# Optimization experiments

Hardware: AMD Instinct MI355X
Metric: run time of the kernel (lower is better)

Reference implementation:

```python
import jax, jax.numpy as jnp
import numpy as np

B, Q, L, D_LLM, D_KEYS = 2, 8, 2048, 768, 64
EPS = 1e-5

def setup_inputs() -> dict:
    key = jax.random.key(0)
    ks = jax.random.split(key, 7)
    s_in = 1.0 / np.sqrt(D_LLM)
    return {
        "info": jax.random.normal(ks[0], (B, Q, L, D_LLM), dtype=jnp.float32),
        "Wq": jax.random.uniform(ks[1], (D_LLM, D_KEYS), jnp.float32, -s_in, s_in),
        "bq": jax.random.uniform(ks[2], (D_KEYS,), jnp.float32, -s_in, s_in),
        "Wk": jax.random.uniform(ks[3], (D_LLM, D_KEYS), jnp.float32, -s_in, s_in),
        "bk": jax.random.uniform(ks[4], (D_KEYS,), jnp.float32, -s_in, s_in),
        "Wv": jax.random.uniform(ks[5], (D_LLM, D_KEYS), jnp.float32, -s_in, s_in),
        "bv": jax.random.uniform(ks[6], (D_KEYS,), jnp.float32, -s_in, s_in),
    }

def reference(info, Wq, bq, Wk, bk, Wv, bv):
    # Projections: [B,Q,L,d_llm] @ [d_llm,d_keys] -> [B,Q,L,E]
    q = info @ Wq + bq
    k = info @ Wk + bk
    v = info @ Wv + bv
    E = q.shape[-1]
    scale = 1.0 / jnp.sqrt(jnp.asarray(E, dtype=q.dtype))
    # Full L x L score tensor per (b,q) slice, as in the original einsum path
    scores = jnp.einsum('bqle,bqme->bqlm', q, k)
    A = jax.nn.softmax(scale * scores, axis=-1)  # dropout is identity at eval
    out = jnp.einsum('bqlm,bqme->bqle', A, v)    # [B,Q,L,E]
    # InstanceNorm2d (no affine): normalize each (b,q) slice over (L,E)
    mu = jnp.mean(out, axis=(2, 3), keepdims=True)
    var = jnp.var(out, axis=(2, 3), keepdims=True)  # biased variance
    return (out - mu) / jnp.sqrt(var + EPS)
```

## Files before the change

kernel.cpp:

```cpp
#include <hip/hip_runtime.h>
#include <math.h>

#define L_SEQ   2048
#define DLLM    768
#define E_DIM   64
#define NSLICE  16
#define EPSV    1e-5f

typedef _Float16 f16;
typedef _Float16 f16x8 __attribute__((ext_vector_type(8)));
typedef _Float16 f16x4 __attribute__((ext_vector_type(4)));
typedef float    f32x4 __attribute__((ext_vector_type(4)));

__global__ __launch_bounds__(256)
void prep_kernel(const float* __restrict__ Wq, const float* __restrict__ bq,
                 const float* __restrict__ Wk, const float* __restrict__ bk,
                 const float* __restrict__ Wv, const float* __restrict__ bv,
                 f16* __restrict__ Wt, float* __restrict__ bias)
{
    int b = blockIdx.x;
    if (b < 192) {
        int sel = b >> 6, c = b & 63;
        const float* W = (sel == 0) ? Wq : (sel == 1) ? Wk : Wv;
        float s = (sel == 0) ? 0.125f : 1.0f;
        for (int kd = threadIdx.x; kd < DLLM; kd += 256)
            Wt[b * DLLM + kd] = (f16)(W[kd * 64 + c] * s);
    } else {
        int t = threadIdx.x;
        if (t < 192) {
            int sel = t >> 6, c = t & 63;
            const float* bb = (sel == 0) ? bq : (sel == 1) ? bk : bv;
            bias[t] = bb[c] * ((sel == 0) ? 0.125f : 1.0f);
        }
    }
}

#define PSTR 72

__global__ __launch_bounds__(256)
void proj_mfma(const float* __restrict__ info, const f16* __restrict__ Wt,
               const float* __restrict__ bias,
               f16* __restrict__ q16, f16* __restrict__ k16, f16* __restrict__ v16)
{
    __shared__ f16 As[128 * PSTR];
    __shared__ f16 Bs[192 * PSTR];

    const int tid = threadIdx.x;
    const int l   = tid & 63;
    const int wid = tid >> 6;
    const int l15 = l & 15, lg = l >> 4;
    const int wm  = (wid >> 1) * 64;
    const int wn  = (wid & 1) * 96;
    const int r0  = blockIdx.x * 128;

    f32x4 acc[4][6];
    #pragma unroll
    for (int i = 0; i < 4; ++i)
        #pragma unroll
        for (int j = 0; j < 6; ++j) acc[i][j] = (f32x4)(0.0f);

    for (int k0 = 0; k0 < DLLM; k0 += 64) {
        __syncthreads();
        #pragma unroll
        for (int u = 0; u < 8; ++u) {
            int f = u * 256 + tid;
            int row = f >> 4, c4 = f & 15;
            float4 v = *reinterpret_cast<const float4*>(
                info + (size_t)(r0 + row) * DLLM + k0 + c4 * 4);
            f16x4 h;
            h[0] = (f16)v.x; h[1] = (f16)v.y; h[2] = (f16)v.z; h[3] = (f16)v.w;
            *reinterpret_cast<f16x4*>(&As[row * PSTR + c4 * 4]) = h;
        }
        #pragma unroll
        for (int u = 0; u < 6; ++u) {
            int f = u * 256 + tid;
            int row = f >> 3, c8 = f & 7;
            f16x8 v = *reinterpret_cast<const f16x8*>(Wt + (size_t)row * DLLM + k0 + c8 * 8);
            *reinterpret_cast<f16x8*>(&Bs[row * PSTR + c8 * 8]) = v;
        }
        __syncthreads();

        #pragma unroll
        for (int kf = 0; kf < 2; ++kf) {
            f16x8 af[4], bf[6];
            #pragma unroll
            for (int mi = 0; mi < 4; ++mi)
                af[mi] = *reinterpret_cast<const f16x8*>(
                    &As[(wm + mi * 16 + l15) * PSTR + kf * 32 + lg * 8]);
            #pragma unroll
            for (int ni = 0; ni < 6; ++ni)
                bf[ni] = *reinterpret_cast<const f16x8*>(
                    &Bs[(wn + ni * 16 + l15) * PSTR + kf * 32 + lg * 8]);
            #pragma unroll
            for (int mi = 0; mi < 4; ++mi)
                #pragma unroll
                for (int ni = 0; ni < 6; ++ni)
                    acc[mi][ni] = __builtin_amdgcn_mfma_f32_16x16x32_f16(
                        af[mi], bf[ni], acc[mi][ni], 0, 0, 0);
        }
    }

    #pragma unroll
    for (int ni = 0; ni < 6; ++ni) {
        int n = wn + ni * 16 + l15;
        float bcol = bias[n];
        int sel = n >> 6, cc = n & 63;
        f16* dst = (sel == 0) ? q16 : (sel == 1) ? k16 : v16;
        #pragma unroll
        for (int mi = 0; mi < 4; ++mi)
            #pragma unroll
            for (int rr = 0; rr < 4; ++rr) {
                int row = r0 + wm + mi * 16 + lg * 4 + rr;
                dst[(size_t)row * E_DIM + cc] = (f16)(acc[mi][ni][rr] + bcol);
            }
    }
}

#define VSTR 72

__global__ __launch_bounds__(256)
void attn_mfma(const f16* __restrict__ q16, const f16* __restrict__ k16,
               const f16* __restrict__ v16, float* __restrict__ att)
{
    __shared__ f16 Vt[64 * VSTR];
    __shared__ f16 Pl[4 * 16 * VSTR];

    const int tid = threadIdx.x;
    const int l   = tid & 63;
    const int wid = tid >> 6;
    const int l15 = l & 15, lg = l >> 4;
    const int slice = blockIdx.y;
    const int m0 = blockIdx.x * 64 + wid * 16;
    const f16* qp = q16 + (size_t)slice * L_SEQ * E_DIM;
    const f16* kp = k16 + (size_t)slice * L_SEQ * E_DIM;
    const f16* vp = v16 + (size_t)slice * L_SEQ * E_DIM;
    f16* P = &Pl[wid * 16 * VSTR];

    f16x8 qf[2];
    #pragma unroll
    for (int kf = 0; kf < 2; ++kf)
        qf[kf] = *reinterpret_cast<const f16x8*>(
            qp + (size_t)(m0 + l15) * E_DIM + kf * 32 + lg * 8);

    f32x4 oacc[4];
    #pragma unroll
    for (int ni = 0; ni < 4; ++ni) oacc[ni] = (f32x4)(0.0f);
    float M[4] = {-1e30f, -1e30f, -1e30f, -1e30f};
    float Lr[4] = {0.f, 0.f, 0.f, 0.f};

    for (int kv0 = 0; kv0 < L_SEQ; kv0 += 64) {
        __syncthreads();

        #pragma unroll
        for (int u = 0; u < 2; ++u) {
            int f  = u * 256 + tid;
            int r  = f >> 3;
            int c8 = f & 7;
            f16x8 h = *reinterpret_cast<const f16x8*>(
                vp + (size_t)(kv0 + r) * E_DIM + c8 * 8);
            int col = r ^ (c8 << 3);
            #pragma unroll
            for (int j = 0; j < 8; ++j)
                Vt[(c8 * 8 + j) * VSTR + col] = h[j];
        }

        f32x4 s[4];
        #pragma unroll
        for (int ni = 0; ni < 4; ++ni) s[ni] = (f32x4)(0.0f);
        #pragma unroll
        for (int kf = 0; kf < 2; ++kf)
            #pragma unroll
            for (int ni = 0; ni < 4; ++ni) {
                f16x8 kb = *reinterpret_cast<const f16x8*>(
                    kp + (size_t)(kv0 + ni * 16 + l15) * E_DIM + kf * 32 + lg * 8);
                s[ni] = __builtin_amdgcn_mfma_f32_16x16x32_f16(qf[kf], kb, s[ni], 0, 0, 0);
            }

        #pragma unroll
        for (int r = 0; r < 4; ++r) {
            float v0 = s[0][r], v1 = s[1][r], v2 = s[2][r], v3 = s[3][r];
            float mx = fmaxf(fmaxf(v0, v1), fmaxf(v2, v3));
            mx = fmaxf(mx, __shfl_xor(mx, 1));
            mx = fmaxf(mx, __shfl_xor(mx, 2));
            mx = fmaxf(mx, __shfl_xor(mx, 4));
            mx = fmaxf(mx, __shfl_xor(mx, 8));
            float mn  = fmaxf(M[r], mx);
            float fsc = __expf(M[r] - mn);
            M[r] = mn;
            float p0 = __expf(v0 - mn), p1 = __expf(v1 - mn);
            float p2 = __expf(v2 - mn), p3 = __expf(v3 - mn);
            int prow = (lg * 4 + r) * VSTR + l15;
            P[prow +  0] = (f16)p0;
            P[prow + 16] = (f16)p1;
            P[prow + 32] = (f16)p2;
            P[prow + 48] = (f16)p3;
            Lr[r] = Lr[r] * fsc + (p0 + p1 + p2 + p3);
            oacc[0][r] *= fsc; oacc[1][r] *= fsc;
            oacc[2][r] *= fsc; oacc[3][r] *= fsc;
        }

        __syncthreads();

        #pragma unroll
        for (int kf = 0; kf < 2; ++kf) {
            f16x8 pa = *reinterpret_cast<const f16x8*>(
                &P[l15 * VSTR + kf * 32 + lg * 8]);
            #pragma unroll
            for (int ni = 0; ni < 4; ++ni) {
                int e   = ni * 16 + l15;
                int col = (kf * 32 + lg * 8) ^ ((e >> 3) << 3);
                f16x8 vb = *reinterpret_cast<const f16x8*>(&Vt[e * VSTR + col]);
                oacc[ni] = __builtin_amdgcn_mfma_f32_16x16x32_f16(pa, vb, oacc[ni], 0, 0, 0);
            }
        }
    }

    #pragma unroll
    for (int r = 0; r < 4; ++r) {
        float lt = Lr[r];
        lt += __shfl_xor(lt, 1);
        lt += __shfl_xor(lt, 2);
        lt += __shfl_xor(lt, 4);
        lt += __shfl_xor(lt, 8);
        float inv = 1.f / lt;
        size_t row = (size_t)slice * L_SEQ + m0 + lg * 4 + r;
        #pragma unroll
        for (int ni = 0; ni < 4; ++ni)
            att[row * E_DIM + ni * 16 + l15] = oacc[ni][r] * inv;
    }
}

__global__ __launch_bounds__(256)
void stats_kernel(const float* __restrict__ att, float* __restrict__ parts)
{
    const int slice = blockIdx.x >> 4;
    const int part  = blockIdx.x & 15;
    const int tid = threadIdx.x;
    const size_t base = (size_t)slice * L_SEQ * E_DIM + (size_t)part * 8192;
    float s = 0.f, sq = 0.f;
    #pragma unroll
    for (int it = 0; it < 8; ++it) {
        float4 v = *reinterpret_cast<const float4*>(att + base + (size_t)(it * 256 + tid) * 4);
        s  += v.x + v.y + v.z + v.w;
        sq += v.x * v.x + v.y * v.y + v.z * v.z + v.w * v.w;
    }
    for (int m = 1; m < 64; m <<= 1) {
        s  += __shfl_xor(s,  m);
        sq += __shfl_xor(sq, m);
    }
    __shared__ float red[8];
    const int wid = tid >> 6;
    if ((tid & 63) == 0) { red[wid * 2] = s; red[wid * 2 + 1] = sq; }
    __syncthreads();
    if (tid == 0) {
        parts[slice * 32 + part * 2]     = red[0] + red[2] + red[4] + red[6];
        parts[slice * 32 + part * 2 + 1] = red[1] + red[3] + red[5] + red[7];
    }
}

__global__ __launch_bounds__(256)
void apply_kernel(float* __restrict__ att, const float* __restrict__ parts)
{
    const int i4 = blockIdx.x * 256 + threadIdx.x;
    const size_t fl = (size_t)i4 * 4;
    const int slice = (int)(fl >> 17);
    float S = 0.f, SQ = 0.f;
    #pragma unroll
    for (int p = 0; p < 16; ++p) {
        S  += parts[slice * 32 + p * 2];
        SQ += parts[slice * 32 + p * 2 + 1];
    }
    const float N = (float)(L_SEQ * E_DIM);
    float mean = S / N;
    float var  = SQ / N - mean * mean;
    float inv  = rsqrtf(var + EPSV);
    float4 v = *reinterpret_cast<const float4*>(att + fl);
    float4 o;
    o.x = (v.x - mean) * inv;
    o.y = (v.y - mean) * inv;
    o.z = (v.z - mean) * inv;
    o.w = (v.w - mean) * inv;
    *reinterpret_cast<float4*>(att + fl) = o;
}

extern "C" void kernel_launch(void* const* d_in, const int* in_sizes, int n_in,
                              void* d_out, int out_size, void* d_ws, size_t ws_size,
                              hipStream_t stream)
{
    const float* info = (const float*)d_in[0];
    const float* Wq   = (const float*)d_in[1];
    const float* bq   = (const float*)d_in[2];
    const float* Wk   = (const float*)d_in[3];
    const float* bk   = (const float*)d_in[4];
    const float* Wv   = (const float*)d_in[5];
    const float* bv   = (const float*)d_in[6];

    char* ws = (char*)d_ws;
    f16*   Wt    = (f16*)(ws);
    float* bias  = (float*)(ws + 294912);
    float* parts = (float*)(ws + 295936);
    f16*   q16   = (f16*)(ws + 1048576);
    f16*   k16   = (f16*)(ws + 5242880);
    f16*   v16   = (f16*)(ws + 9437184);
    float* att   = (float*)d_out;

    prep_kernel<<<193, 256, 0, stream>>>(Wq, bq, Wk, bk, Wv, bv, Wt, bias);
    proj_mfma<<<256, 256, 0, stream>>>(info, Wt, bias, q16, k16, v16);
    attn_mfma<<<dim3(L_SEQ / 64, NSLICE), 256, 0, stream>>>(q16, k16, v16, att);
    stats_kernel<<<256, 256, 0, stream>>>(att, parts);
    apply_kernel<<<2048, 256, 0, stream>>>(att, parts);
}
```

Baseline: 270.8 us.

## Store V transposed, drop LDS staging and block syncs, register-prefetch projection

```diff
diff --git a/kernel.cpp b/kernel.cpp
--- a/kernel.cpp
+++ b/kernel.cpp
@@ -35,135 +35,151 @@
     }
 }
 
-#define PSTR 72
-
 __global__ __launch_bounds__(256)
 void proj_mfma(const float* __restrict__ info, const f16* __restrict__ Wt,
                const float* __restrict__ bias,
-               f16* __restrict__ q16, f16* __restrict__ k16, f16* __restrict__ v16)
-{
-    __shared__ f16 As[128 * PSTR];
-    __shared__ f16 Bs[192 * PSTR];
-
+               f16* __restrict__ q16, f16* __restrict__ k16, f16* __restrict__ vT)
+{
     const int tid = threadIdx.x;
     const int l   = tid & 63;
     const int wid = tid >> 6;
     const int l15 = l & 15, lg = l >> 4;
-    const int wm  = (wid >> 1) * 64;
-    const int wn  = (wid & 1) * 96;
-    const int r0  = blockIdx.x * 128;
-
-    f32x4 acc[4][6];
-    #pragma unroll
-    for (int i = 0; i < 4; ++i)
-        #pragma unroll
-        for (int j = 0; j < 6; ++j) acc[i][j] = (f32x4)(0.0f);
-
-    for (int k0 = 0; k0 < DLLM; k0 += 64) {
-        __syncthreads();
-        #pragma unroll
-        for (int u = 0; u < 8; ++u) {
-            int f = u * 256 + tid;
-            int row = f >> 4, c4 = f & 15;
-            float4 v = *reinterpret_cast<const float4*>(
-                info + (size_t)(r0 + row) * DLLM + k0 + c4 * 4);
-            f16x4 h;
-            h[0] = (f16)v.x; h[1] = (f16)v.y; h[2] = (f16)v.z; h[3] = (f16)v.w;
-            *reinterpret_cast<f16x4*>(&As[row * PSTR + c4 * 4]) = h;
-        }
-        #pragma unroll
-        for (int u = 0; u < 6; ++u) {
-            int f = u * 256 + tid;
-            int row = f >> 3, c8 = f & 7;
-            f16x8 v = *reinterpret_cast<const f16x8*>(Wt + (size_t)row * DLLM + k0 + c8 * 8);
-            *reinterpret_cast<f16x8*>(&Bs[row * PSTR + c8 * 8]) = v;
-        }
-        __syncthreads();
-
+    const int w   = blockIdx.x * 4 + wid;
+    const int rt  = w >> 1;
+    const int ch  = w & 1;
+    const int r0  = rt * 32;
+    const int n0  = ch * 96;
+
+    f32x4 acc[2][6];
+    #pragma unroll
+    for (int mi = 0; mi < 2; ++mi)
+        #pragma unroll
+        for (int ni = 0; ni < 6; ++ni) acc[mi][ni] = (f32x4)(0.0f);
+
+    const float* abase[2];
+    #pragma unroll
+    for (int mi = 0; mi < 2; ++mi)
+        abase[mi] = info + (size_t)(r0 + mi * 16 + l15) * DLLM + lg * 8;
+    const f16* bbase[6];
+    #pragma unroll
+    for (int ni = 0; ni < 6; ++ni)
+        bbase[ni] = Wt + (size_t)(n0 + ni * 16 + l15) * DLLM + lg * 8;
+
+    float4 alo[2][2][2], ahi[2][2][2];
+
+    #pragma unroll
+    for (int mi = 0; mi < 2; ++mi)
         #pragma unroll
         for (int kf = 0; kf < 2; ++kf) {
-            f16x8 af[4], bf[6];
-            #pragma unroll
-            for (int mi = 0; mi < 4; ++mi)
-                af[mi] = *reinterpret_cast<const f16x8*>(
-                    &As[(wm + mi * 16 + l15) * PSTR + kf * 32 + lg * 8]);
-            #pragma unroll
-            for (int ni = 0; ni < 6; ++ni)
-                bf[ni] = *reinterpret_cast<const f16x8*>(
-                    &Bs[(wn + ni * 16 + l15) * PSTR + kf * 32 + lg * 8]);
-            #pragma unroll
-            for (int mi = 0; mi < 4; ++mi)
+            alo[0][mi][kf] = *reinterpret_cast<const float4*>(abase[mi] + kf * 32);
+            ahi[0][mi][kf] = *reinterpret_cast<const float4*>(abase[mi] + kf * 32 + 4);
+        }
+
+    #pragma unroll
+    for (int ks = 0; ks < 12; ++ks) {
+        const int cur = ks & 1, nxt = cur ^ 1;
+        const int k0 = ks * 64;
+        if (ks < 11) {
+            #pragma unroll
+            for (int mi = 0; mi < 2; ++mi)
+                #pragma unroll
+                for (int kf = 0; kf < 2; ++kf) {
+                    alo[nxt][mi][kf] = *reinterpret_cast<const float4*>(
+                        abase[mi] + k0 + 64 + kf * 32);
+                    ahi[nxt][mi][kf] = *reinterpret_cast<const float4*>(
+                        abase[mi] + k0 + 64 + kf * 32 + 4);
+                }
+        }
+        f16x8 bf[6][2];
+        #pragma unroll
+        for (int ni = 0; ni < 6; ++ni)
+            #pragma unroll
+            for (int kf = 0; kf < 2; ++kf)
+                bf[ni][kf] = *reinterpret_cast<const f16x8*>(bbase[ni] + k0 + kf * 32);
+        f16x8 af[2][2];
+        #pragma unroll
+        for (int mi = 0; mi < 2; ++mi)
+            #pragma unroll
+            for (int kf = 0; kf < 2; ++kf) {
+                float4 lo = alo[cur][mi][kf], hi = ahi[cur][mi][kf];
+                f16x8 h;
+                h[0] = (f16)lo.x; h[1] = (f16)lo.y; h[2] = (f16)lo.z; h[3] = (f16)lo.w;
+                h[4] = (f16)hi.x; h[5] = (f16)hi.y; h[6] = (f16)hi.z; h[7] = (f16)hi.w;
+                af[mi][kf] = h;
+            }
+        #pragma unroll
+        for (int kf = 0; kf < 2; ++kf)
+            #pragma unroll
+            for (int mi = 0; mi < 2; ++mi)
                 #pragma unroll
                 for (int ni = 0; ni < 6; ++ni)
                     acc[mi][ni] = __builtin_amdgcn_mfma_f32_16x16x32_f16(
-                        af[mi], bf[ni], acc[mi][ni], 0, 0, 0);
-        }
+                        af[mi][kf], bf[ni][kf], acc[mi][ni], 0, 0, 0);
     }
 
     #pragma unroll
     for (int ni = 0; ni < 6; ++ni) {
-        int n = wn + ni * 16 + l15;
-        float bcol = bias[n];
-        int sel = n >> 6, cc = n & 63;
-        f16* dst = (sel == 0) ? q16 : (sel == 1) ? k16 : v16;
-        #pragma unroll
-        for (int mi = 0; mi < 4; ++mi)
-            #pragma unroll
-            for (int rr = 0; rr < 4; ++rr) {
-                int row = r0 + wm + mi * 16 + lg * 4 + rr;
-                dst[(size_t)row * E_DIM + cc] = (f16)(acc[mi][ni][rr] + bcol);
-            }
-    }
-}
-
-#define VSTR 72
+        const int nb  = n0 + ni * 16;
+        const int n   = nb + l15;
+        const int sel = nb >> 6;
+        const int cc  = (nb & 63) + l15;
+        const float bcol = bias[n];
+        if (sel < 2) {
+            f16* dst = (sel == 0) ? q16 : k16;
+            #pragma unroll
+            for (int mi = 0; mi < 2; ++mi)
+                #pragma unroll
+                for (int rr = 0; rr < 4; ++rr) {
+                    int r = r0 + mi * 16 + lg * 4 + rr;
+                    dst[(size_t)r * E_DIM + cc] = (f16)(acc[mi][ni][rr] + bcol);
+                }
+        } else {
+            #pragma unroll
+            for (int mi = 0; mi < 2; ++mi) {
+                int rb    = r0 + mi * 16 + lg * 4;
+                int slice = rb >> 11;
+                int lloc  = rb & 2047;
+                f16x4 v4;
+                #pragma unroll
+                for (int rr = 0; rr < 4; ++rr) v4[rr] = (f16)(acc[mi][ni][rr] + bcol);
+                *reinterpret_cast<f16x4*>(
+                    vT + (size_t)slice * E_DIM * L_SEQ + (size_t)cc * L_SEQ + lloc) = v4;
+            }
+        }
+    }
+}
+
+#define PSTRD 72
 
 __global__ __launch_bounds__(256)
 void attn_mfma(const f16* __restrict__ q16, const f16* __restrict__ k16,
-               const f16* __restrict__ v16, float* __restrict__ att)
-{
-    __shared__ f16 Vt[64 * VSTR];
-    __shared__ f16 Pl[4 * 16 * VSTR];
+               const f16* __restrict__ vT, float* __restrict__ att)
+{
+    __shared__ f16 Pl[4 * 16 * PSTRD];
 
     const int tid = threadIdx.x;
     const int l   = tid & 63;
     const int wid = tid >> 6;
     const int l15 = l & 15, lg = l >> 4;
     const int slice = blockIdx.y;
-    const int m0 = blockIdx.x * 64 + wid * 16;
+    const int q0 = blockIdx.x * 64 + wid * 16;
     const f16* qp = q16 + (size_t)slice * L_SEQ * E_DIM;
     const f16* kp = k16 + (size_t)slice * L_SEQ * E_DIM;
-    const f16* vp = v16 + (size_t)slice * L_SEQ * E_DIM;
-    f16* P = &Pl[wid * 16 * VSTR];
+    const f16* vp = vT  + (size_t)slice * E_DIM * L_SEQ;
+    f16* P = &Pl[wid * 16 * PSTRD];
 
     f16x8 qf[2];
     #pragma unroll
     for (int kf = 0; kf < 2; ++kf)
         qf[kf] = *reinterpret_cast<const f16x8*>(
-            qp + (size_t)(m0 + l15) * E_DIM + kf * 32 + lg * 8);
+            qp + (size_t)(q0 + l15) * E_DIM + kf * 32 + lg * 8);
 
     f32x4 oacc[4];
     #pragma unroll
-    for (int ni = 0; ni < 4; ++ni) oacc[ni] = (f32x4)(0.0f);
-    float M[4] = {-1e30f, -1e30f, -1e30f, -1e30f};
-    float Lr[4] = {0.f, 0.f, 0.f, 0.f};
+    for (int ei = 0; ei < 4; ++ei) oacc[ei] = (f32x4)(0.0f);
+    float M = -1e30f, Lr = 0.f;
 
     for (int kv0 = 0; kv0 < L_SEQ; kv0 += 64) {
-        __syncthreads();
-
-        #pragma unroll
-        for (int u = 0; u < 2; ++u) {
-            int f  = u * 256 + tid;
-            int r  = f >> 3;
-            int c8 = f & 7;
-            f16x8 h = *reinterpret_cast<const f16x8*>(
-                vp + (size_t)(kv0 + r) * E_DIM + c8 * 8);
-            int col = r ^ (c8 << 3);
-            #pragma unroll
-            for (int j = 0; j < 8; ++j)
-                Vt[(c8 * 8 + j) * VSTR + col] = h[j];
-        }
-
         f32x4 s[4];
         #pragma unroll
         for (int ni = 0; ni < 4; ++ni) s[ni] = (f32x4)(0.0f);
@@ -173,60 +189,62 @@
             for (int ni = 0; ni < 4; ++ni) {
                 f16x8 kb = *reinterpret_cast<const f16x8*>(
                     kp + (size_t)(kv0 + ni * 16 + l15) * E_DIM + kf * 32 + lg * 8);
-                s[ni] = __builtin_amdgcn_mfma_f32_16x16x32_f16(qf[kf], kb, s[ni], 0, 0, 0);
-            }
-
-        #pragma unroll
-        for (int r = 0; r < 4; ++r) {
-            float v0 = s[0][r], v1 = s[1][r], v2 = s[2][r], v3 = s[3][r];
-            float mx = fmaxf(fmaxf(v0, v1), fmaxf(v2, v3));
-            mx = fmaxf(mx, __shfl_xor(mx, 1));
-            mx = fmaxf(mx, __shfl_xor(mx, 2));
-            mx = fmaxf(mx, __shfl_xor(mx, 4));
-            mx = fmaxf(mx, __shfl_xor(mx, 8));
-            float mn  = fmaxf(M[r], mx);
-            float fsc = __expf(M[r] - mn);
-            M[r] = mn;
-            float p0 = __expf(v0 - mn), p1 = __expf(v1 - mn);
-            float p2 = __expf(v2 - mn), p3 = __expf(v3 - mn);
-            int prow = (lg * 4 + r) * VSTR + l15;
-            P[prow +  0] = (f16)p0;
-            P[prow + 16] = (f16)p1;
-            P[prow + 32] = (f16)p2;
-            P[prow + 48] = (f16)p3;
-            Lr[r] = Lr[r] * fsc + (p0 + p1 + p2 + p3);
-            oacc[0][r] *= fsc; oacc[1][r] *= fsc;
-            oacc[2][r] *= fsc; oacc[3][r] *= fsc;
-        }
-
-        __syncthreads();
+                s[ni] = __builtin_amdgcn_mfma_f32_16x16x32_f16(kb, qf[kf], s[ni], 0, 0, 0);
+            }
+
+        float mx = -1e30f;
+        #pragma unroll
+        for (int ni = 0; ni < 4; ++ni)
+            #pragma unroll
+            for (int r = 0; r < 4; ++r) mx = fmaxf(mx, s[ni][r]);
+        mx = fmaxf(mx, __shfl_xor(mx, 16));
+        mx = fmaxf(mx, __shfl_xor(mx, 32));
+        float Mn  = fmaxf(M, mx);
+        float fsc = __expf(M - Mn);
+        M = Mn;
+        float psum = 0.f;
+        #pragma unroll
+        for (int ni = 0; ni < 4; ++ni) {
+            f16x4 p4;
+            #pragma unroll
+            for (int r = 0; r < 4; ++r) {
+                float p = __expf(s[ni][r] - Mn);
+                psum += p;
+                p4[r] = (f16)p;
+            }
+            *reinterpret_cast<f16x4*>(&P[l15 * PSTRD + ni * 16 + lg * 4]) = p4;
+        }
+        Lr = Lr * fsc + psum;
+        #pragma unroll
+        for (int ei = 0; ei < 4; ++ei) {
+            oacc[ei][0] *= fsc; oacc[ei][1] *= fsc;
+            oacc[ei][2] *= fsc; oacc[ei][3] *= fsc;
+        }
 
         #pragma unroll
         for (int kf = 0; kf < 2; ++kf) {
             f16x8 pa = *reinterpret_cast<const f16x8*>(
-                &P[l15 * VSTR + kf * 32 + lg * 8]);
-            #pragma unroll
-            for (int ni = 0; ni < 4; ++ni) {
-                int e   = ni * 16 + l15;
-                int col = (kf * 32 + lg * 8) ^ ((e >> 3) << 3);
-                f16x8 vb = *reinterpret_cast<const f16x8*>(&Vt[e * VSTR + col]);
-                oacc[ni] = __builtin_amdgcn_mfma_f32_16x16x32_f16(pa, vb, oacc[ni], 0, 0, 0);
-            }
-        }
-    }
-
-    #pragma unroll
-    for (int r = 0; r < 4; ++r) {
-        float lt = Lr[r];
-        lt += __shfl_xor(lt, 1);
-        lt += __shfl_xor(lt, 2);
-        lt += __shfl_xor(lt, 4);
-        lt += __shfl_xor(lt, 8);
-        float inv = 1.f / lt;
-        size_t row = (size_t)slice * L_SEQ + m0 + lg * 4 + r;
-        #pragma unroll
-        for (int ni = 0; ni < 4; ++ni)
-            att[row * E_DIM + ni * 16 + l15] = oacc[ni][r] * inv;
+                &P[l15 * PSTRD + kf * 32 + lg * 8]);
+            #pragma unroll
+            for (int ei = 0; ei < 4; ++ei) {
+                f16x8 vb = *reinterpret_cast<const f16x8*>(
+                    vp + (size_t)(ei * 16 + l15) * L_SEQ + kv0 + kf * 32 + lg * 8);
+                oacc[ei] = __builtin_amdgcn_mfma_f32_16x16x32_f16(vb, pa, oacc[ei], 0, 0, 0);
+            }
+        }
+    }
+
+    float lt = Lr;
+    lt += __shfl_xor(lt, 16);
+    lt += __shfl_xor(lt, 32);
+    float inv = 1.f / lt;
+    size_t row = (size_t)slice * L_SEQ + q0 + l15;
+    #pragma unroll
+    for (int ei = 0; ei < 4; ++ei) {
+        float4 o;
+        o.x = oacc[ei][0] * inv; o.y = oacc[ei][1] * inv;
+        o.z = oacc[ei][2] * inv; o.w = oacc[ei][3] * inv;
+        *reinterpret_cast<float4*>(att + row * E_DIM + ei * 16 + lg * 4) = o;
     }
 }
 
@@ -301,12 +319,12 @@
     float* parts = (float*)(ws + 295936);
     f16*   q16   = (f16*)(ws + 1048576);
     f16*   k16   = (f16*)(ws + 5242880);
-    f16*   v16   = (f16*)(ws + 9437184);
+    f16*   vT    = (f16*)(ws + 9437184);
     float* att   = (float*)d_out;
 
     prep_kernel<<<193, 256, 0, stream>>>(Wq, bq, Wk, bk, Wv, bv, Wt, bias);
-    proj_mfma<<<256, 256, 0, stream>>>(info, Wt, bias, q16, k16, v16);
-    attn_mfma<<<dim3(L_SEQ / 64, NSLICE), 256, 0, stream>>>(q16, k16, v16, att);
+    proj_mfma<<<512, 256, 0, stream>>>(info, Wt, bias, q16, k16, vT);
+    attn_mfma<<<dim3(L_SEQ / 64, NSLICE), 256, 0, stream>>>(q16, k16, vT, att);
     stats_kernel<<<256, 256, 0, stream>>>(att, parts);
     apply_kernel<<<2048, 256, 0, stream>>>(att, parts);
 }
```

New measurement: 328.6 us. +21.3%, slower.
